# Performance work log

Hardware: AMD Instinct MI355X
Metric: run time of the kernel (lower is better)

The kernel has to match this reference:

```python
import jax, jax.numpy as jnp
import numpy as np


def setup_inputs() -> dict:
    key = jax.random.key(0)
    ks = jax.random.split(key, 12)
    B, C, H, W = 8, 512, 48, 48
    HW = H * W
    inp = {
        'key': jax.random.normal(ks[0], (B, C, H, W), dtype=jnp.float32),
        'sds': jax.random.uniform(ks[1], (B, HW, H, W), dtype=jnp.float32),
        'global_bg': jax.random.normal(ks[2], (B, HW, C), dtype=jnp.float32),
        'global_fg': jax.random.normal(ks[3], (B, HW, C), dtype=jnp.float32),
        'local_bg': jax.random.normal(ks[4], (B, HW, C), dtype=jnp.float32),
        'local_fg': jax.random.normal(ks[5], (B, HW, C), dtype=jnp.float32),
        'overall_bg': jax.random.normal(ks[6], (B, 1, C), dtype=jnp.float32),
        'overall_fg': jax.random.normal(ks[7], (B, 1, C), dtype=jnp.float32),
        'short_bg': jax.random.normal(ks[8], (B, 1, C), dtype=jnp.float32),
        'short_fg': jax.random.normal(ks[9], (B, 1, C), dtype=jnp.float32),
        'long_bg': jax.random.normal(ks[10], (B, 1, C), dtype=jnp.float32),
        'long_fg': jax.random.normal(ks[11], (B, 1, C), dtype=jnp.float32),
    }
    return inp


def reference(key, sds, global_bg, global_fg, local_bg, local_fg,
              overall_bg, overall_fg, short_bg, short_fg, long_bg, long_fg):
    B, C, H, W = key.shape
    HW = H * W
    k = key.reshape(B, C, HW)                 # [B, C, HW]
    mask = sds.reshape(B, HW, HW)             # [B, HW(mem), HW(query)]

    def fine_max(bank, m=None):
        # bank: [B, HW, C]; score: [B, HW(mem), HW(query)]
        s = jnp.einsum('bmc,bcn->bmn', bank, k)
        if m is not None:
            s = s * m
        return jnp.max(s, axis=1).reshape(B, 1, H, W)

    def coarse(bank):
        # bank: [B, 1, C]
        return jnp.einsum('boc,bcn->bon', bank, k).reshape(B, 1, H, W)

    global_score = jnp.concatenate([fine_max(global_bg), fine_max(global_fg)], axis=1)
    local_score = jnp.concatenate([fine_max(local_bg, mask), fine_max(local_fg, mask)], axis=1)
    fine_score = jnp.concatenate([global_score, local_score], axis=1)

    coarse_score = jnp.concatenate([
        coarse(overall_bg), coarse(overall_fg),
        coarse(short_bg), coarse(short_fg),
        coarse(long_bg), coarse(long_fg),
    ], axis=1)

    matching_score = jnp.concatenate([fine_score, coarse_score], axis=1)  # [B, 10, H, W]
    return matching_score
```

## Files before the change

### kernel.cpp

```cpp
#include <hip/hip_runtime.h>

#define B_   8
#define C_   512
#define HW_  2304
#define BM   128
#define BN   128
#define BKQ  32
#define NKS  (C_ / BKQ)
#define NT_  (HW_ / BN)
#define MT_PER_BLOCK 3
#define MCHUNKS 6
#define NSTEPS (MT_PER_BLOCK * NKS)
#define TILE_SH (BM * BKQ)
#define BUF_SH  (3 * TILE_SH)

typedef __bf16 bf16x8 __attribute__((ext_vector_type(8)));
typedef float  f32x4  __attribute__((ext_vector_type(4)));

__device__ __forceinline__ unsigned short f2bf(float f) {
  unsigned int u = __float_as_uint(f);
  u += 0x7FFF + ((u >> 16) & 1);
  return (unsigned short)(u >> 16);
}

__device__ __forceinline__ void gload_lds16(const void* g, void* l) {
  __builtin_amdgcn_global_load_lds(
      (const __attribute__((address_space(1))) unsigned int*)g,
      (__attribute__((address_space(3))) unsigned int*)l, 16, 0, 0);
}

__global__ void zero_out(float* __restrict__ out, int n) {
  int i = blockIdx.x * 256 + threadIdx.x;
  if (i < n) out[i] = 0.0f;
}

__global__ void transpose_coarse(const float* __restrict__ key,
                                 const float* __restrict__ v0, const float* __restrict__ v1,
                                 const float* __restrict__ v2, const float* __restrict__ v3,
                                 const float* __restrict__ v4, const float* __restrict__ v5,
                                 unsigned short* __restrict__ keyT,
                                 float* __restrict__ out) {
  __shared__ float tile[32][33];
  __shared__ float red2[6][8][32];
  int b  = blockIdx.z;
  int n0 = blockIdx.x * 32;
  int c0 = blockIdx.y * 32;
  int tx = threadIdx.x;
  int ty = threadIdx.y;
#pragma unroll
  for (int i = 0; i < 4; i++) {
    int c = c0 + ty + i * 8;
    tile[ty + i * 8][tx] = key[(size_t)b * C_ * HW_ + (size_t)c * HW_ + n0 + tx];
  }
  __syncthreads();
#pragma unroll
  for (int i = 0; i < 4; i++) {
    int n = n0 + ty + i * 8;
    keyT[(size_t)b * HW_ * C_ + (size_t)n * C_ + c0 + tx] = f2bf(tile[tx][ty + i * 8]);
  }
  float s[6] = {0.f, 0.f, 0.f, 0.f, 0.f, 0.f};
#pragma unroll
  for (int i = 0; i < 4; i++) {
    int cr = ty * 4 + i;
    int c  = c0 + cr;
    float kv = tile[cr][tx];
    s[0] += v0[b * C_ + c] * kv;
    s[1] += v1[b * C_ + c] * kv;
    s[2] += v2[b * C_ + c] * kv;
    s[3] += v3[b * C_ + c] * kv;
    s[4] += v4[b * C_ + c] * kv;
    s[5] += v5[b * C_ + c] * kv;
  }
#pragma unroll
  for (int j = 0; j < 6; j++) red2[j][ty][tx] = s[j];
  __syncthreads();
  if (ty < 6) {
    float a = 0.f;
#pragma unroll
    for (int k = 0; k < 8; k++) a += red2[ty][k][tx];
    atomicAdd(&out[((size_t)b * 10 + 4 + ty) * HW_ + n0 + tx], a);
  }
}

__global__ void convert_banks(const float* __restrict__ b0, const float* __restrict__ b1,
                              const float* __restrict__ b2, const float* __restrict__ b3,
                              unsigned short* __restrict__ out) {
  const size_t per = (size_t)B_ * HW_ * C_;
  int g = blockIdx.y;
  const float* src = (g == 0) ? b0 : (g == 1) ? b1 : (g == 2) ? b2 : b3;
  size_t i = ((size_t)blockIdx.x * blockDim.x + threadIdx.x) * 4;
  float4 v = *(const float4*)(src + i);
  ushort4 o;
  o.x = f2bf(v.x); o.y = f2bf(v.y); o.z = f2bf(v.z); o.w = f2bf(v.w);
  *(ushort4*)(out + g * per + i) = o;
}

__global__ __launch_bounds__(512, 3) void fine_kernel(
    const unsigned short* __restrict__ keyT,
    const unsigned short* __restrict__ banks,
    const float* __restrict__ sds,
    float* __restrict__ pmax) {
  int lin = blockIdx.x;
  int b   = lin & 7;
  int ix  = lin >> 3;
  int gp  = (ix >= 108) ? 1 : 0;
  int w   = ix - gp * 108;
  int mc  = w / NT_;
  int nt  = w % NT_;
  int n0  = nt * BN;

  __shared__ __align__(16) unsigned short sbuf[3][3][TILE_SH];
  __shared__ float red[8][64];

  int t    = threadIdx.x;
  int wave = t >> 6;
  int lane = t & 63;
  int quad = lane >> 4;
  int l15  = lane & 15;
  int bank_i = wave & 1;
  int wm   = ((wave >> 1) & 1) * 64;
  int wn   = (wave >> 2) * 64;

  int rbase = wave * 16;
  int ksub  = (lane & 3) ^ ((lane >> 3) & 3);
  int swo   = (quad ^ ((l15 >> 1) & 3)) * 8;

  const unsigned short* bank0 = banks + ((size_t)(2 * gp) * B_ + b) * (size_t)HW_ * C_;
  const unsigned short* bank1 = banks + ((size_t)(2 * gp + 1) * B_ + b) * (size_t)HW_ * C_;
  const unsigned short* keyb  = keyT + (size_t)b * HW_ * C_;
  const float* maskb = sds + (size_t)b * HW_ * HW_;
  const bool masked = (gp == 1);

  size_t lane_off = (size_t)(rbase + (lane >> 2)) * C_ + (size_t)ksub * 8;
  const unsigned short* a0p = bank0 + (size_t)mc * MT_PER_BLOCK * BM * C_ + lane_off;
  const unsigned short* a1p = bank1 + (size_t)mc * MT_PER_BLOCK * BM * C_ + lane_off;
  const unsigned short* kbp = keyb  + (size_t)n0 * C_ + lane_off;

  auto STAGE = [&](int P, int s) {
    int offA = ((s >> 4) << 16) + ((s & 15) << 5);
    int offB = (s & 15) << 5;
    unsigned short* dst = &sbuf[0][0][0] + P * BUF_SH + rbase * BKQ;
    gload_lds16(a0p + offA, dst);
    gload_lds16(a1p + offA, dst + TILE_SH);
    gload_lds16(kbp + offB, dst + 2 * TILE_SH);
  };

  float rm[4];
#pragma unroll
  for (int i = 0; i < 4; i++) rm[i] = -3.4e38f;

  STAGE(0, 0);
  STAGE(1, 1);

  for (int mi = 0; mi < MT_PER_BLOCK; mi++) {
    f32x4 acc[4][4];
#pragma unroll
    for (int i = 0; i < 4; i++)
#pragma unroll
      for (int j = 0; j < 4; j++)
#pragma unroll
        for (int e = 0; e < 4; e++) acc[i][j][e] = 0.0f;

    for (int kc = 0; kc < NKS; kc++) {
      int s = (mi << 4) | kc;
      if (s < NSTEPS - 1) asm volatile("s_waitcnt vmcnt(3)" ::: "memory");
      else                asm volatile("s_waitcnt vmcnt(0)" ::: "memory");
      __builtin_amdgcn_s_barrier();
      int sn = s + 2;
      if (sn < NSTEPS) STAGE(sn % 3, sn);

      const unsigned short* base  = &sbuf[0][0][0] + (s % 3) * BUF_SH;
      const unsigned short* Abase = base + bank_i * TILE_SH;
      const unsigned short* Bbase = base + 2 * TILE_SH;
      bf16x8 a[4], bv[4];
#pragma unroll
      for (int ms = 0; ms < 4; ms++)
        a[ms] = *(const bf16x8*)(Abase + (wm + ms * 16 + l15) * BKQ + swo);
#pragma unroll
      for (int ns = 0; ns < 4; ns++)
        bv[ns] = *(const bf16x8*)(Bbase + (wn + ns * 16 + l15) * BKQ + swo);
      asm volatile("s_waitcnt lgkmcnt(0)" ::: "memory");
      __builtin_amdgcn_sched_barrier(0);

      __builtin_amdgcn_s_setprio(1);
#pragma unroll
      for (int ms = 0; ms < 4; ms++)
#pragma unroll
        for (int ns = 0; ns < 4; ns++)
          acc[ms][ns] = __builtin_amdgcn_mfma_f32_16x16x32_bf16(
              a[ms], bv[ns], acc[ms][ns], 0, 0, 0);
      __builtin_amdgcn_s_setprio(0);
    }

    int m0 = (mc * MT_PER_BLOCK + mi) * BM;
#pragma unroll
    for (int ms = 0; ms < 4; ms++) {
#pragma unroll
      for (int ns = 0; ns < 4; ns++) {
        int n = n0 + wn + ns * 16 + l15;
#pragma unroll
        for (int r = 0; r < 4; r++) {
          int m = m0 + wm + ms * 16 + quad * 4 + r;
          float s0 = acc[ms][ns][r];
          if (masked) {
            float w_ = maskb[(size_t)m * HW_ + n];
            s0 *= w_;
          }
          rm[ns] = fmaxf(rm[ns], s0);
        }
      }
    }
  }

#pragma unroll
  for (int ns = 0; ns < 4; ns++) {
    float v = rm[ns];
    v = fmaxf(v, __shfl_xor(v, 16, 64));
    v = fmaxf(v, __shfl_xor(v, 32, 64));
    rm[ns] = v;
  }
  if (lane < 16) {
#pragma unroll
    for (int ns = 0; ns < 4; ns++) red[wave][ns * 16 + l15] = rm[ns];
  }
  __syncthreads();
  if (t < 256) {
    int bank = t >> 7;
    int nn   = t & 127;
    int wnh  = nn >> 6;
    int nl   = nn & 63;
    float v = fmaxf(red[bank + wnh * 4][nl], red[bank + 2 + wnh * 4][nl]);
    pmax[(((size_t)mc * B_ + b) * 4 + 2 * gp + bank) * HW_ + n0 + nn] = v;
  }
}

__global__ void fine_combine(const float* __restrict__ pmax, float* __restrict__ out) {
  int i = blockIdx.x * 256 + threadIdx.x;
  if (i >= B_ * 4 * HW_) return;
  int n = i % HW_;
  int g = (i / HW_) % 4;
  int b = i / (HW_ * 4);
  float v = -3.4e38f;
#pragma unroll
  for (int mc = 0; mc < MCHUNKS; mc++)
    v = fmaxf(v, pmax[(((size_t)mc * B_ + b) * 4 + g) * HW_ + n]);
  out[((size_t)b * 10 + g) * HW_ + n] = v;
}

extern "C" void kernel_launch(void* const* d_in, const int* in_sizes, int n_in,
                              void* d_out, int out_size, void* d_ws, size_t ws_size,
                              hipStream_t stream) {
  const float* key  = (const float*)d_in[0];
  const float* sds  = (const float*)d_in[1];
  const float* gbg  = (const float*)d_in[2];
  const float* gfg  = (const float*)d_in[3];
  const float* lbg  = (const float*)d_in[4];
  const float* lfg  = (const float*)d_in[5];
  const float* obg  = (const float*)d_in[6];
  const float* ofg  = (const float*)d_in[7];
  const float* sbg  = (const float*)d_in[8];
  const float* sfg  = (const float*)d_in[9];
  const float* lobg = (const float*)d_in[10];
  const float* lofg = (const float*)d_in[11];
  float* out = (float*)d_out;

  unsigned short* keyT  = (unsigned short*)d_ws;
  unsigned short* banks = keyT + (size_t)B_ * HW_ * C_;
  float* pmax = (float*)(banks + (size_t)4 * B_ * HW_ * C_);

  zero_out<<<(out_size + 255) / 256, 256, 0, stream>>>(out, out_size);
  convert_banks<<<dim3((B_ * HW_ * C_) / (4 * 256), 4), 256, 0, stream>>>(gbg, gfg, lbg, lfg, banks);
  transpose_coarse<<<dim3(HW_ / 32, C_ / 32, B_), dim3(32, 8), 0, stream>>>(
      key, obg, ofg, sbg, sfg, lobg, lofg, keyT, out);
  fine_kernel<<<dim3(NT_ * MCHUNKS * 2 * B_), 512, 0, stream>>>(keyT, banks, sds, pmax);
  fine_combine<<<(B_ * 4 * HW_ + 255) / 256, 256, 0, stream>>>(pmax, out);
}
```

Before: 827.7 us.

## Split fine kernel into one bank per block with 128x64 tiles

```diff
diff --git a/kernel.cpp b/kernel.cpp
--- a/kernel.cpp
+++ b/kernel.cpp
@@ -4,15 +4,16 @@
 #define C_   512
 #define HW_  2304
 #define BM   128
-#define BN   128
+#define BN   64
 #define BKQ  32
 #define NKS  (C_ / BKQ)
 #define NT_  (HW_ / BN)
 #define MT_PER_BLOCK 3
 #define MCHUNKS 6
 #define NSTEPS (MT_PER_BLOCK * NKS)
-#define TILE_SH (BM * BKQ)
-#define BUF_SH  (3 * TILE_SH)
+#define TILE_A_SH (BM * BKQ)
+#define TILE_B_SH (BN * BKQ)
+#define BUF_SH    (TILE_A_SH + TILE_B_SH)
 
 typedef __bf16 bf16x8 __attribute__((ext_vector_type(8)));
 typedef float  f32x4  __attribute__((ext_vector_type(4)));
@@ -95,69 +96,65 @@
   *(ushort4*)(out + g * per + i) = o;
 }
 
-__global__ __launch_bounds__(512, 3) void fine_kernel(
+__global__ __launch_bounds__(256, 4) void fine_kernel(
     const unsigned short* __restrict__ keyT,
     const unsigned short* __restrict__ banks,
     const float* __restrict__ sds,
     float* __restrict__ pmax) {
   int lin = blockIdx.x;
   int b   = lin & 7;
-  int ix  = lin >> 3;
-  int gp  = (ix >= 108) ? 1 : 0;
-  int w   = ix - gp * 108;
-  int mc  = w / NT_;
-  int nt  = w % NT_;
+  int r   = lin >> 3;
+  int mc  = r / (NT_ * 4);
+  int r2  = r % (NT_ * 4);
+  int nt  = r2 >> 2;
+  int g   = r2 & 3;
   int n0  = nt * BN;
 
-  __shared__ __align__(16) unsigned short sbuf[3][3][TILE_SH];
-  __shared__ float red[8][64];
+  __shared__ __align__(16) unsigned short sbuf[3][BUF_SH];
+  __shared__ float red[4][32];
 
   int t    = threadIdx.x;
   int wave = t >> 6;
   int lane = t & 63;
   int quad = lane >> 4;
   int l15  = lane & 15;
-  int bank_i = wave & 1;
-  int wm   = ((wave >> 1) & 1) * 64;
-  int wn   = (wave >> 2) * 64;
-
-  int rbase = wave * 16;
-  int ksub  = (lane & 3) ^ ((lane >> 3) & 3);
-  int swo   = (quad ^ ((l15 >> 1) & 3)) * 8;
-
-  const unsigned short* bank0 = banks + ((size_t)(2 * gp) * B_ + b) * (size_t)HW_ * C_;
-  const unsigned short* bank1 = banks + ((size_t)(2 * gp + 1) * B_ + b) * (size_t)HW_ * C_;
+  int wm   = (wave & 1) * 64;
+  int wn   = (wave >> 1) * 32;
+
+  int ksub = (lane & 3) ^ ((lane >> 3) & 3);
+  int swo  = (quad ^ ((l15 >> 1) & 3)) * 8;
+
+  const unsigned short* bankg = banks + ((size_t)g * B_ + b) * (size_t)HW_ * C_;
   const unsigned short* keyb  = keyT + (size_t)b * HW_ * C_;
   const float* maskb = sds + (size_t)b * HW_ * HW_;
-  const bool masked = (gp == 1);
-
-  size_t lane_off = (size_t)(rbase + (lane >> 2)) * C_ + (size_t)ksub * 8;
-  const unsigned short* a0p = bank0 + (size_t)mc * MT_PER_BLOCK * BM * C_ + lane_off;
-  const unsigned short* a1p = bank1 + (size_t)mc * MT_PER_BLOCK * BM * C_ + lane_off;
-  const unsigned short* kbp = keyb  + (size_t)n0 * C_ + lane_off;
+  const bool masked = (g >= 2);
+
+  size_t laneA = (size_t)(wave * 32 + (lane >> 2)) * C_ + (size_t)ksub * 8;
+  size_t laneB = (size_t)(wave * 16 + (lane >> 2)) * C_ + (size_t)ksub * 8;
+  const unsigned short* a0p = bankg + (size_t)mc * MT_PER_BLOCK * BM * C_ + laneA;
+  const unsigned short* kbp = keyb + (size_t)n0 * C_ + laneB;
 
   auto STAGE = [&](int P, int s) {
     int offA = ((s >> 4) << 16) + ((s & 15) << 5);
     int offB = (s & 15) << 5;
-    unsigned short* dst = &sbuf[0][0][0] + P * BUF_SH + rbase * BKQ;
-    gload_lds16(a0p + offA, dst);
-    gload_lds16(a1p + offA, dst + TILE_SH);
-    gload_lds16(kbp + offB, dst + 2 * TILE_SH);
+    unsigned short* dst = &sbuf[P][0];
+    gload_lds16(a0p + offA,           dst + (wave * 32) * BKQ);
+    gload_lds16(a0p + offA + 16 * C_, dst + (wave * 32 + 16) * BKQ);
+    gload_lds16(kbp + offB,           dst + TILE_A_SH + (wave * 16) * BKQ);
   };
 
-  float rm[4];
-#pragma unroll
-  for (int i = 0; i < 4; i++) rm[i] = -3.4e38f;
+  float rm[2];
+  rm[0] = -3.4e38f; rm[1] = -3.4e38f;
 
   STAGE(0, 0);
   STAGE(1, 1);
 
   for (int mi = 0; mi < MT_PER_BLOCK; mi++) {
-    f32x4 acc[4][4];
+    f32x4 acc[4][2];
 #pragma unroll
     for (int i = 0; i < 4; i++)
 #pragma unroll
-      for (int j = 0; j < 4; j++)
+      for (int j = 0; j < 2; j++)
 #pragma unroll
         for (int e = 0; e < 4; e++) acc[i][j][e] = 0.0f;
 
@@ -169,15 +166,14 @@
       int sn = s + 2;
       if (sn < NSTEPS) STAGE(sn % 3, sn);
 
-      const unsigned short* base  = &sbuf[0][0][0] + (s % 3) * BUF_SH;
-      const unsigned short* Abase = base + bank_i * TILE_SH;
-      const unsigned short* Bbase = base + 2 * TILE_SH;
-      bf16x8 a[4], bv[4];
+      const unsigned short* Abase = &sbuf[s % 3][0];
+      const unsigned short* Bbase = Abase + TILE_A_SH;
+      bf16x8 a[4], bv[2];
 #pragma unroll
       for (int ms = 0; ms < 4; ms++)
         a[ms] = *(const bf16x8*)(Abase + (wm + ms * 16 + l15) * BKQ + swo);
 #pragma unroll
-      for (int ns = 0; ns < 4; ns++)
+      for (int ns = 0; ns < 2; ns++)
         bv[ns] = *(const bf16x8*)(Bbase + (wn + ns * 16 + l15) * BKQ + swo);
       asm volatile("s_waitcnt lgkmcnt(0)" ::: "memory");
       __builtin_amdgcn_sched_barrier(0);
@@ -186,7 +182,7 @@
 #pragma unroll
       for (int ms = 0; ms < 4; ms++)
 #pragma unroll
-        for (int ns = 0; ns < 4; ns++)
+        for (int ns = 0; ns < 2; ns++)
           acc[ms][ns] = __builtin_amdgcn_mfma_f32_16x16x32_bf16(
               a[ms], bv[ns], acc[ms][ns], 0, 0, 0);
       __builtin_amdgcn_s_setprio(0);
@@ -196,12 +192,12 @@
 #pragma unroll
     for (int ms = 0; ms < 4; ms++) {
 #pragma unroll
-      for (int ns = 0; ns < 4; ns++) {
+      for (int ns = 0; ns < 2; ns++) {
         int n = n0 + wn + ns * 16 + l15;
 #pragma unroll
-        for (int r = 0; r < 4; r++) {
-          int m = m0 + wm + ms * 16 + quad * 4 + r;
-          float s0 = acc[ms][ns][r];
+        for (int rr = 0; rr < 4; rr++) {
+          int m = m0 + wm + ms * 16 + quad * 4 + rr;
+          float s0 = acc[ms][ns][rr];
           if (masked) {
             float w_ = maskb[(size_t)m * HW_ + n];
             s0 *= w_;
@@ -213,7 +209,7 @@
   }
 
 #pragma unroll
-  for (int ns = 0; ns < 4; ns++) {
+  for (int ns = 0; ns < 2; ns++) {
     float v = rm[ns];
     v = fmaxf(v, __shfl_xor(v, 16, 64));
     v = fmaxf(v, __shfl_xor(v, 32, 64));
@@ -221,16 +217,14 @@
   }
   if (lane < 16) {
 #pragma unroll
-    for (int ns = 0; ns < 4; ns++) red[wave][ns * 16 + l15] = rm[ns];
+    for (int ns = 0; ns < 2; ns++) red[wave][ns * 16 + l15] = rm[ns];
   }
   __syncthreads();
-  if (t < 256) {
-    int bank = t >> 7;
-    int nn   = t & 127;
-    int wnh  = nn >> 6;
-    int nl   = nn & 63;
-    float v = fmaxf(red[bank + wnh * 4][nl], red[bank + 2 + wnh * 4][nl]);
-    pmax[(((size_t)mc * B_ + b) * 4 + 2 * gp + bank) * HW_ + n0 + nn] = v;
+  if (t < BN) {
+    int wnh = t >> 5;
+    int nl  = t & 31;
+    float v = fmaxf(red[2 * wnh][nl], red[2 * wnh + 1][nl]);
+    pmax[(((size_t)mc * B_ + b) * 4 + g) * HW_ + n0 + t] = v;
   }
 }
 
@@ -272,6 +266,6 @@
   convert_banks<<<dim3((B_ * HW_ * C_) / (4 * 256), 4), 256, 0, stream>>>(gbg, gfg, lbg, lfg, banks);
   transpose_coarse<<<dim3(HW_ / 32, C_ / 32, B_), dim3(32, 8), 0, stream>>>(
       key, obg, ofg, sbg, sfg, lobg, lofg, keyT, out);
-  fine_kernel<<<dim3(NT_ * MCHUNKS * 2 * B_), 512, 0, stream>>>(keyT, banks, sds, pmax);
+  fine_kernel<<<dim3(MCHUNKS * NT_ * 4 * B_), 256, 0, stream>>>(keyT, banks, sds, pmax);
   fine_combine<<<(B_ * 4 * HW_ + 255) / 256, 256, 0, stream>>>(pmax, out);
 }
```

New measurement: 795.9 us. 3.8% less time.
